# Optimization experiments

Hardware: AMD Instinct MI355X
Metric: run time of the kernel (lower is better)

Reference implementation:

```python
import jax, jax.numpy as jnp
import numpy as np

D_HEAD = 64

def setup_inputs() -> dict:
    key = jax.random.key(0)
    kq, kk, kv, kc = jax.random.split(key, 4)
    B, H, T, D = 2, 16, 2048, D_HEAD
    Q = jax.random.normal(kq, (B, H, T, D), dtype=jnp.float32)
    K = jax.random.normal(kk, (B, H, T, D), dtype=jnp.float32)
    V = jax.random.normal(kv, (B, H, T, D), dtype=jnp.float32)
    # causal mask: True = attend
    mask = jnp.tril(jnp.ones((T, T), dtype=jnp.bool_))
    curvature = jax.random.normal(kc, (H, D, D), dtype=jnp.float32) * 0.02
    return {"Q": Q, "K": K, "V": V, "mask": mask, "curvature": curvature}

def reference(Q, K, V, mask, curvature):
    scale = 1.0 / np.sqrt(Q.shape[-1]).astype(np.float32)
    # per-head learned rotation of Q
    Q_rot = jnp.einsum('bhtd,hde->bhte', Q, curvature)
    scores = jnp.einsum('bhtd,bhsd->bhts', Q_rot, K) * scale  # [B,H,T,T]
    scores = jnp.where(mask[None, None, :, :], scores, -jnp.inf)
    attn = jax.nn.softmax(scores, axis=-1)
    out = jnp.einsum('bhts,bhsd->bhtd', attn, V)
    return out
```

## Files before the change

kernel.cpp:

```cpp
#include <hip/hip_runtime.h>


typedef __attribute__((ext_vector_type(8))) short short8;
typedef __attribute__((ext_vector_type(8))) unsigned short ushort8;
typedef __attribute__((ext_vector_type(4))) float f32x4;
typedef __attribute__((ext_vector_type(2))) _Float16 half2v;
typedef __attribute__((ext_vector_type(4))) _Float16 half4;
typedef __attribute__((ext_vector_type(8))) _Float16 half8;

constexpr int Tc = 2048;
constexpr int Dc = 64;
constexpr size_t REGION = (size_t)32 * Tc * Dc;

__device__ inline unsigned short f2bf(float f) {
    union { float f; unsigned u; } x; x.f = f;
    return (unsigned short)((x.u + 0x7fffu + ((x.u >> 16) & 1u)) >> 16);
}

__device__ inline half2v pkrtz(float a, float b) {
    return __builtin_bit_cast(half2v, __builtin_amdgcn_cvt_pkrtz(a, b));
}

#define MFMA_BF16_K32(a, b, c) __builtin_amdgcn_mfma_f32_16x16x32_bf16((a), (b), (c), 0, 0, 0)
#define MFMA_F16_K16(a, b, c)  __builtin_amdgcn_mfma_f32_16x16x16f16((a), (b), (c), 0, 0, 0)

__global__ __launch_bounds__(256, 1)
void holo_cfrag(const float* __restrict__ Cp, unsigned short* __restrict__ cfrag_g)
{
    const int t = threadIdx.x, lane = t & 63, eb = t >> 6;
    const int l15 = lane & 15, quad = lane >> 4;
    const int h = blockIdx.x;
    const float* Cg = Cp + (size_t)h * Dc * Dc;
    #pragma unroll
    for (int half = 0; half < 2; ++half) {
        short8 b;
        #pragma unroll
        for (int jj = 0; jj < 8; ++jj) {
            const int d = half * 32 + quad * 8 + jj;
            b[jj] = (short)f2bf(Cg[d * Dc + eb * 16 + l15]);
        }
        *(short8*)(&cfrag_g[(((size_t)h * 4 + eb) * 2 + half) * 512 + lane * 8]) = b;
    }
}

__global__ __launch_bounds__(256, 4)
void holo_prep8(const float* __restrict__ Qp, const float* __restrict__ Kp,
                const float* __restrict__ Vp,
                const unsigned short* __restrict__ cfrag_g,
                unsigned short* __restrict__ qfrag_g,
                unsigned short* __restrict__ kfrag_g,
                _Float16* __restrict__ vfrag_g)
{
    __shared__ unsigned short kt[64 * 72];
    __shared__ unsigned short qt[64 * 72];
    __shared__ _Float16      vt[64 * 72];
    __shared__ unsigned short pf[64 * 72];

    const int t = threadIdx.x, lane = t & 63, w = t >> 6;
    const int l15 = lane & 15, quad = lane >> 4, wb = w * 16;
    const int n = blockIdx.x, bh = n >> 5, st = n & 31, h = bh & 15;
    const int s0 = st * 64;

    const float* Qg = Qp + ((size_t)bh * Tc + s0) * Dc;
    const float* Kg = Kp + ((size_t)bh * Tc + s0) * Dc;
    const float* Vg = Vp + ((size_t)bh * Tc + s0) * Dc;

    #pragma unroll
    for (int kk = 0; kk < 4; ++kk) {
        const int flat = kk * 1024 + t * 4;
        const int r = flat >> 6, d0 = flat & 63;
        float4 kv = *(const float4*)(&Kg[flat]);
        ushort4 kp; kp.x = f2bf(kv.x); kp.y = f2bf(kv.y); kp.z = f2bf(kv.z); kp.w = f2bf(kv.w);
        *(ushort4*)(&kt[r * 72 + d0]) = kp;
        float4 qv = *(const float4*)(&Qg[flat]);
        ushort4 qp; qp.x = f2bf(qv.x); qp.y = f2bf(qv.y); qp.z = f2bf(qv.z); qp.w = f2bf(qv.w);
        *(ushort4*)(&qt[r * 72 + d0]) = qp;
        float4 vv = *(const float4*)(&Vg[flat]);
        half4 vp;
        vp[0] = (_Float16)vv.x; vp[1] = (_Float16)vv.y;
        vp[2] = (_Float16)vv.z; vp[3] = (_Float16)vv.w;
        *(half4*)(&vt[r * 72 + d0]) = vp;
    }
    __syncthreads();

    {
        const int row = wb + l15;
        ushort8 p0 = *(const ushort8*)(&kt[row * 72 + quad * 8]);
        ushort8 p1 = *(const ushort8*)(&kt[row * 72 + 32 + quad * 8]);
        unsigned short* kdst = kfrag_g + (((size_t)(bh * 32 + st) * 4 + w) * 64 + lane) * 16;
        *(ushort8*)(kdst) = p0;
        *(ushort8*)(kdst + 8) = p1;
    }

    {
        half8 v0, v1;
        #pragma unroll
        for (int dn = 0; dn < 2; ++dn)
            #pragma unroll
            for (int i = 0; i < 4; ++i)
                v0[dn * 4 + i] = vt[(wb + quad * 4 + i) * 72 + dn * 16 + l15];
        #pragma unroll
        for (int dn = 0; dn < 2; ++dn)
            #pragma unroll
            for (int i = 0; i < 4; ++i)
                v1[dn * 4 + i] = vt[(wb + quad * 4 + i) * 72 + (dn + 2) * 16 + l15];
        _Float16* vdst = vfrag_g + (((size_t)(bh * 32 + st) * 4 + w) * 64 + lane) * 16;
        *(half8*)(vdst) = v0;
        *(half8*)(vdst + 8) = v1;
    }

    {
        short8 a0 = *(const short8*)(&qt[(wb + l15) * 72 + quad * 8]);
        short8 a1 = *(const short8*)(&qt[(wb + l15) * 72 + 32 + quad * 8]);
        #pragma unroll
        for (int eb = 0; eb < 4; ++eb) {
            short8 b0 = *(const short8*)(&cfrag_g[(((size_t)h * 4 + eb) * 2 + 0) * 512 + lane * 8]);
            short8 b1 = *(const short8*)(&cfrag_g[(((size_t)h * 4 + eb) * 2 + 1) * 512 + lane * 8]);
            f32x4 c = {0.f, 0.f, 0.f, 0.f};
            c = MFMA_BF16_K32(a0, b0, c);
            c = MFMA_BF16_K32(a1, b1, c);
            #pragma unroll
            for (int i = 0; i < 4; ++i)
                pf[(wb + quad * 4 + i) * 72 + eb * 16 + l15] = f2bf(c[i] * 0.18033688f);
        }
        __threadfence_block();
        short8 fa0 = *(const short8*)(&pf[(wb + l15) * 72 + quad * 8]);
        short8 fa1 = *(const short8*)(&pf[(wb + l15) * 72 + 32 + quad * 8]);
        const size_t strip = (size_t)bh * 128 + st * 4 + w;
        *(short8*)(&qfrag_g[strip * 1024 + lane * 8]) = fa0;
        *(short8*)(&qfrag_g[strip * 1024 + 512 + lane * 8]) = fa1;
    }
}

__global__ __launch_bounds__(256, 4)
void holo_attn8(const unsigned short* __restrict__ qfrag_g,
                const unsigned short* __restrict__ kfrag_g,
                const _Float16* __restrict__ vfrag_g,
                float* __restrict__ Op)
{
    const int t = threadIdx.x, lane = t & 63, wid = t >> 6;
    const int l15 = lane & 15, quad = lane >> 4, wb = wid * 16;

    const int id = blockIdx.x;
    const int xcd = id & 7, m = (id >> 3) & 31, k = id >> 8;
    const int bh = xcd * 4 + k;
    const int mm = (k >= 2) ? ((m + 16) & 31) : m;
    const int qi = (k & 1) ? (31 - mm) : mm;
    const int q0 = qi * 64;

    short8 qa0, qa1;
    {
        const size_t strip = (size_t)bh * 128 + qi * 4 + wid;
        qa0 = *(const short8*)(&qfrag_g[strip * 1024 + lane * 8]);
        qa1 = *(const short8*)(&qfrag_g[strip * 1024 + 512 + lane * 8]);
    }

    const unsigned short* kbase = kfrag_g + (size_t)bh * 32 * 4 * 1024;
    const _Float16*       vbase = vfrag_g + (size_t)bh * 32 * 4 * 1024;

    f32x4 o[4];
    float l_lane = 0.f;
    #pragma unroll
    for (int dn = 0; dn < 4; ++dn) o[dn] = f32x4{0.f, 0.f, 0.f, 0.f};

    const int rowg = q0 + wb + l15;

    short8 kf0[4], kf1[4];
    half8 vlo[4], vhi[4];
    #pragma unroll
    for (int tn = 0; tn < 4; ++tn) {
        const unsigned short* kfb = kbase + ((size_t)tn * 64 + lane) * 16;
        kf0[tn] = *(const short8*)(kfb);
        kf1[tn] = *(const short8*)(kfb + 8);
        const _Float16* vfb = vbase + ((size_t)tn * 64 + lane) * 16;
        vlo[tn] = *(const half8*)(vfb);
        vhi[tn] = *(const half8*)(vfb + 8);
    }

    for (int j = 0; j <= qi; ++j) {
        f32x4 st[4];
        #pragma unroll
        for (int tn = 0; tn < 4; ++tn) {
            f32x4 c = {0.f, 0.f, 0.f, 0.f};
            c = MFMA_BF16_K32(kf0[tn], qa0, c);
            c = MFMA_BF16_K32(kf1[tn], qa1, c);
            st[tn] = c;
        }

        const int jn = (j < qi) ? j + 1 : j;
        #pragma unroll
        for (int tn = 0; tn < 4; ++tn) {
            const unsigned short* kfb = kbase + (size_t)jn * 4096 + ((size_t)tn * 64 + lane) * 16;
            kf0[tn] = *(const short8*)(kfb);
            kf1[tn] = *(const short8*)(kfb + 8);
        }

        half4 pa[4];
        #pragma unroll
        for (int tn = 0; tn < 4; ++tn) {
            float p[4];
            #pragma unroll
            for (int i = 0; i < 4; ++i) {
                float sv = st[tn][i];
                if (j == qi) {
                    const int colg = j * 64 + tn * 16 + quad * 4 + i;
                    if (colg > rowg) sv = -1e30f;
                }
                p[i] = __builtin_amdgcn_exp2f(sv);
                l_lane += p[i];
            }
            half2v lo = pkrtz(p[0], p[1]);
            half2v hi = pkrtz(p[2], p[3]);
            pa[tn] = __builtin_shufflevector(lo, hi, 0, 1, 2, 3);
        }

        #pragma unroll
        for (int tn = 0; tn < 4; ++tn) {
            half4 vf0 = __builtin_shufflevector(vlo[tn], vlo[tn], 0, 1, 2, 3);
            half4 vf1 = __builtin_shufflevector(vlo[tn], vlo[tn], 4, 5, 6, 7);
            half4 vf2 = __builtin_shufflevector(vhi[tn], vhi[tn], 0, 1, 2, 3);
            half4 vf3 = __builtin_shufflevector(vhi[tn], vhi[tn], 4, 5, 6, 7);
            o[0] = MFMA_F16_K16(vf0, pa[tn], o[0]);
            o[1] = MFMA_F16_K16(vf1, pa[tn], o[1]);
            o[2] = MFMA_F16_K16(vf2, pa[tn], o[2]);
            o[3] = MFMA_F16_K16(vf3, pa[tn], o[3]);
        }

        #pragma unroll
        for (int tn = 0; tn < 4; ++tn) {
            const _Float16* vfb = vbase + (size_t)jn * 4096 + ((size_t)tn * 64 + lane) * 16;
            vlo[tn] = *(const half8*)(vfb);
            vhi[tn] = *(const half8*)(vfb + 8);
        }
    }

    l_lane += __shfl_xor(l_lane, 16);
    l_lane += __shfl_xor(l_lane, 32);
    const float inv = 1.0f / l_lane;

    float* dst = Op + ((size_t)bh * Tc + rowg) * Dc;
    #pragma unroll
    for (int dn = 0; dn < 4; ++dn) {
        float4 r;
        r.x = o[dn][0] * inv; r.y = o[dn][1] * inv;
        r.z = o[dn][2] * inv; r.w = o[dn][3] * inv;
        *(float4*)(&dst[dn * 16 + quad * 4]) = r;
    }
}

extern "C" void kernel_launch(void* const* d_in, const int* in_sizes, int n_in,
                              void* d_out, int out_size, void* d_ws, size_t ws_size,
                              hipStream_t stream) {
    const float* Q = (const float*)d_in[0];
    const float* K = (const float*)d_in[1];
    const float* V = (const float*)d_in[2];
    const float* C = (const float*)d_in[4];
    float* O = (float*)d_out;

    unsigned short* qfrag_w = (unsigned short*)d_ws;
    unsigned short* kfrag_w = qfrag_w + REGION;
    _Float16*       vfrag_w = (_Float16*)(kfrag_w + REGION);
    unsigned short* cfrag_w = (unsigned short*)(vfrag_w + REGION);

    holo_cfrag<<<dim3(16), dim3(256), 0, stream>>>(C, cfrag_w);
    holo_prep8<<<dim3(1024), dim3(256), 0, stream>>>(Q, K, V, cfrag_w, qfrag_w, kfrag_w, vfrag_w);
    holo_attn8<<<dim3(1024), dim3(256), 0, stream>>>(qfrag_w, kfrag_w, vfrag_w, O);
}
```

Before: 144.6 us.

## Split KV loop across wave pairs, two query strips per wave, LDS merge

The attention kernel is restructured so each wave handles two 16-row query strips, with K/V fragment loads shared between them. The four waves form two parity groups, one taking even KV tiles and one taking odd tiles, and the partial outputs and row sums are merged through LDS at the end. Blocks are also reordered longest-first (qi counts down), and launch bounds drop to 2 blocks per SIMD because register use rises. The goal is to halve K/V loads per query row and shorten each wave's serial loop, at the cost of more registers, lower occupancy and a final sync and LDS reduction.

Result: faster. 136.9 us (-5.3%).

```diff
diff --git a/kernel.cpp b/kernel.cpp
--- a/kernel.cpp
+++ b/kernel.cpp
@@ -132,62 +132,74 @@
     }
 }
 
-__global__ __launch_bounds__(256, 4)
-void holo_attn8(const unsigned short* __restrict__ qfrag_g,
-                const unsigned short* __restrict__ kfrag_g,
-                const _Float16* __restrict__ vfrag_g,
-                float* __restrict__ Op)
+__global__ __launch_bounds__(256, 2)
+void holo_attn10(const unsigned short* __restrict__ qfrag_g,
+                 const unsigned short* __restrict__ kfrag_g,
+                 const _Float16* __restrict__ vfrag_g,
+                 float* __restrict__ Op)
 {
+    __shared__ float lds_o[2][2][16][68];
+    __shared__ float lds_l[2][2][16];
+
     const int t = threadIdx.x, lane = t & 63, wid = t >> 6;
-    const int l15 = lane & 15, quad = lane >> 4, wb = wid * 16;
+    const int l15 = lane & 15, quad = lane >> 4;
+    const int hv  = wid & 1;
+    const int par = wid >> 1;
 
     const int id = blockIdx.x;
-    const int xcd = id & 7, m = (id >> 3) & 31, k = id >> 8;
-    const int bh = xcd * 4 + k;
-    const int mm = (k >= 2) ? ((m + 16) & 31) : m;
-    const int qi = (k & 1) ? (31 - mm) : mm;
+    const int xcd = id & 7, sseq = id >> 3;
+    const int qi = 31 - (sseq >> 2);
+    const int bh = xcd * 4 + (sseq & 3);
     const int q0 = qi * 64;
 
-    short8 qa0, qa1;
-    {
-        const size_t strip = (size_t)bh * 128 + qi * 4 + wid;
-        qa0 = *(const short8*)(&qfrag_g[strip * 1024 + lane * 8]);
-        qa1 = *(const short8*)(&qfrag_g[strip * 1024 + 512 + lane * 8]);
+    short8 qa0[2], qa1[2];
+    #pragma unroll
+    for (int s2 = 0; s2 < 2; ++s2) {
+        const size_t strip = (size_t)bh * 128 + qi * 4 + (2 * hv + s2);
+        qa0[s2] = *(const short8*)(&qfrag_g[strip * 1024 + lane * 8]);
+        qa1[s2] = *(const short8*)(&qfrag_g[strip * 1024 + 512 + lane * 8]);
     }
 
     const unsigned short* kbase = kfrag_g + (size_t)bh * 32 * 4 * 1024;
     const _Float16*       vbase = vfrag_g + (size_t)bh * 32 * 4 * 1024;
 
-    f32x4 o[4];
-    float l_lane = 0.f;
-    #pragma unroll
-    for (int dn = 0; dn < 4; ++dn) o[dn] = f32x4{0.f, 0.f, 0.f, 0.f};
-
-    const int rowg = q0 + wb + l15;
+    f32x4 o[2][4];
+    #pragma unroll
+    for (int s2 = 0; s2 < 2; ++s2)
+        #pragma unroll
+        for (int dn = 0; dn < 4; ++dn) o[s2][dn] = f32x4{0.f, 0.f, 0.f, 0.f};
+    float l2[2] = {0.f, 0.f};
+
+    const int rowgA = q0 + (2 * hv) * 16 + l15;
+    const int rowgB = rowgA + 16;
 
     short8 kf0[4], kf1[4];
     half8 vlo[4], vhi[4];
     #pragma unroll
     for (int tn = 0; tn < 4; ++tn) {
-        const unsigned short* kfb = kbase + ((size_t)tn * 64 + lane) * 16;
+        const unsigned short* kfb = kbase + (size_t)par * 4096 + ((size_t)tn * 64 + lane) * 16;
         kf0[tn] = *(const short8*)(kfb);
         kf1[tn] = *(const short8*)(kfb + 8);
-        const _Float16* vfb = vbase + ((size_t)tn * 64 + lane) * 16;
+        const _Float16* vfb = vbase + (size_t)par * 4096 + ((size_t)tn * 64 + lane) * 16;
         vlo[tn] = *(const half8*)(vfb);
         vhi[tn] = *(const half8*)(vfb + 8);
     }
 
-    for (int j = 0; j <= qi; ++j) {
-        f32x4 st[4];
-        #pragma unroll
-        for (int tn = 0; tn < 4; ++tn) {
-            f32x4 c = {0.f, 0.f, 0.f, 0.f};
-            c = MFMA_BF16_K32(kf0[tn], qa0, c);
-            c = MFMA_BF16_K32(kf1[tn], qa1, c);
-            st[tn] = c;
-        }
-
-        const int jn = (j < qi) ? j + 1 : j;
+    for (int j = par; j <= qi; j += 2) {
+        f32x4 stA[4], stB[4];
+        #pragma unroll
+        for (int tn = 0; tn < 4; ++tn) {
+            f32x4 cA = {0.f, 0.f, 0.f, 0.f};
+            cA = MFMA_BF16_K32(kf0[tn], qa0[0], cA);
+            cA = MFMA_BF16_K32(kf1[tn], qa1[0], cA);
+            stA[tn] = cA;
+            f32x4 cB = {0.f, 0.f, 0.f, 0.f};
+            cB = MFMA_BF16_K32(kf0[tn], qa0[1], cB);
+            cB = MFMA_BF16_K32(kf1[tn], qa1[1], cB);
+            stB[tn] = cB;
+        }
+
+        const int jn = (j + 2 <= qi) ? j + 2 : j;
         #pragma unroll
         for (int tn = 0; tn < 4; ++tn) {
             const unsigned short* kfb = kbase + (size_t)jn * 4096 + ((size_t)tn * 64 + lane) * 16;
@@ -195,23 +207,27 @@
             kf1[tn] = *(const short8*)(kfb + 8);
         }
 
-        half4 pa[4];
-        #pragma unroll
-        for (int tn = 0; tn < 4; ++tn) {
-            float p[4];
+        half4 paA[4], paB[4];
+        #pragma unroll
+        for (int tn = 0; tn < 4; ++tn) {
+            float pA[4], pB[4];
             #pragma unroll
             for (int i = 0; i < 4; ++i) {
-                float sv = st[tn][i];
+                float svA = stA[tn][i], svB = stB[tn][i];
                 if (j == qi) {
                     const int colg = j * 64 + tn * 16 + quad * 4 + i;
-                    if (colg > rowg) sv = -1e30f;
+                    if (colg > rowgA) svA = -1e30f;
+                    if (colg > rowgB) svB = -1e30f;
                 }
-                p[i] = __builtin_amdgcn_exp2f(sv);
-                l_lane += p[i];
+                pA[i] = __builtin_amdgcn_exp2f(svA);
+                pB[i] = __builtin_amdgcn_exp2f(svB);
+                l2[0] += pA[i];
+                l2[1] += pB[i];
             }
-            half2v lo = pkrtz(p[0], p[1]);
-            half2v hi = pkrtz(p[2], p[3]);
-            pa[tn] = __builtin_shufflevector(lo, hi, 0, 1, 2, 3);
+            half2v loA = pkrtz(pA[0], pA[1]), hiA = pkrtz(pA[2], pA[3]);
+            paA[tn] = __builtin_shufflevector(loA, hiA, 0, 1, 2, 3);
+            half2v loB = pkrtz(pB[0], pB[1]), hiB = pkrtz(pB[2], pB[3]);
+            paB[tn] = __builtin_shufflevector(loB, hiB, 0, 1, 2, 3);
         }
 
         #pragma unroll
@@ -220,10 +236,14 @@
             half4 vf1 = __builtin_shufflevector(vlo[tn], vlo[tn], 4, 5, 6, 7);
             half4 vf2 = __builtin_shufflevector(vhi[tn], vhi[tn], 0, 1, 2, 3);
             half4 vf3 = __builtin_shufflevector(vhi[tn], vhi[tn], 4, 5, 6, 7);
-            o[0] = MFMA_F16_K16(vf0, pa[tn], o[0]);
-            o[1] = MFMA_F16_K16(vf1, pa[tn], o[1]);
-            o[2] = MFMA_F16_K16(vf2, pa[tn], o[2]);
-            o[3] = MFMA_F16_K16(vf3, pa[tn], o[3]);
+            o[0][0] = MFMA_F16_K16(vf0, paA[tn], o[0][0]);
+            o[0][1] = MFMA_F16_K16(vf1, paA[tn], o[0][1]);
+            o[0][2] = MFMA_F16_K16(vf2, paA[tn], o[0][2]);
+            o[0][3] = MFMA_F16_K16(vf3, paA[tn], o[0][3]);
+            o[1][0] = MFMA_F16_K16(vf0, paB[tn], o[1][0]);
+            o[1][1] = MFMA_F16_K16(vf1, paB[tn], o[1][1]);
+            o[1][2] = MFMA_F16_K16(vf2, paB[tn], o[1][2]);
+            o[1][3] = MFMA_F16_K16(vf3, paB[tn], o[1][3]);
         }
 
         #pragma unroll
@@ -234,17 +254,43 @@
         }
     }
 
-    l_lane += __shfl_xor(l_lane, 16);
-    l_lane += __shfl_xor(l_lane, 32);
-    const float inv = 1.0f / l_lane;
-
-    float* dst = Op + ((size_t)bh * Tc + rowg) * Dc;
-    #pragma unroll
-    for (int dn = 0; dn < 4; ++dn) {
-        float4 r;
-        r.x = o[dn][0] * inv; r.y = o[dn][1] * inv;
-        r.z = o[dn][2] * inv; r.w = o[dn][3] * inv;
-        *(float4*)(&dst[dn * 16 + quad * 4]) = r;
+    #pragma unroll
+    for (int s2 = 0; s2 < 2; ++s2) {
+        l2[s2] += __shfl_xor(l2[s2], 16);
+        l2[s2] += __shfl_xor(l2[s2], 32);
+    }
+
+    if (par == 1) {
+        #pragma unroll
+        for (int s2 = 0; s2 < 2; ++s2) {
+            #pragma unroll
+            for (int dn = 0; dn < 4; ++dn) {
+                float4 r;
+                r.x = o[s2][dn][0]; r.y = o[s2][dn][1];
+                r.z = o[s2][dn][2]; r.w = o[s2][dn][3];
+                *(float4*)(&lds_o[hv][s2][l15][dn * 16 + quad * 4]) = r;
+            }
+            if (quad == 0) lds_l[hv][s2][l15] = l2[s2];
+        }
+    }
+    __syncthreads();
+    if (par == 0) {
+        #pragma unroll
+        for (int s2 = 0; s2 < 2; ++s2) {
+            const float inv = 1.0f / (l2[s2] + lds_l[hv][s2][l15]);
+            const int rowg = q0 + (2 * hv + s2) * 16 + l15;
+            float* dst = Op + ((size_t)bh * Tc + rowg) * Dc;
+            const float* po = &lds_o[hv][s2][l15][0];
+            #pragma unroll
+            for (int dn = 0; dn < 4; ++dn) {
+                float4 r;
+                r.x = (o[s2][dn][0] + po[dn * 16 + quad * 4 + 0]) * inv;
+                r.y = (o[s2][dn][1] + po[dn * 16 + quad * 4 + 1]) * inv;
+                r.z = (o[s2][dn][2] + po[dn * 16 + quad * 4 + 2]) * inv;
+                r.w = (o[s2][dn][3] + po[dn * 16 + quad * 4 + 3]) * inv;
+                *(float4*)(&dst[dn * 16 + quad * 4]) = r;
+            }
+        }
     }
 }
 
@@ -264,5 +310,5 @@
 
     holo_cfrag<<<dim3(16), dim3(256), 0, stream>>>(C, cfrag_w);
     holo_prep8<<<dim3(1024), dim3(256), 0, stream>>>(Q, K, V, cfrag_w, qfrag_w, kfrag_w, vfrag_w);
-    holo_attn8<<<dim3(1024), dim3(256), 0, stream>>>(qfrag_w, kfrag_w, vfrag_w, O);
-}
+    holo_attn10<<<dim3(1024), dim3(256), 0, stream>>>(qfrag_w, kfrag_w, vfrag_w, O);
+}
```

## Stage K/V tiles through double-buffered LDS via direct global-to-LDS loads

Applied to the files above, without the earlier changes.

The attention kernel now has all four waves of a block share K/V tiles. Each tile is loaded once per block into a double-buffered LDS ring with global_load_lds, instead of every wave loading its own copy into registers. The prep kernel's fragment layout is rearranged so each 16-byte lane load maps contiguously into LDS. Blocks are reordered to schedule the longest causal rows first, and MFMA sections get raised wave priority. The cost is an added barrier and vmcnt wait every iteration plus 32KB of LDS per block, and launch bounds drop to 2 blocks per CU.

Result: faster. 136.7 us (-5.5%).

```diff
diff --git a/kernel.cpp b/kernel.cpp
--- a/kernel.cpp
+++ b/kernel.cpp
@@ -23,6 +23,12 @@
 
 #define MFMA_BF16_K32(a, b, c) __builtin_amdgcn_mfma_f32_16x16x32_bf16((a), (b), (c), 0, 0, 0)
 #define MFMA_F16_K16(a, b, c)  __builtin_amdgcn_mfma_f32_16x16x16f16((a), (b), (c), 0, 0, 0)
+
+typedef __attribute__((address_space(3))) unsigned int        lds_u32;
+typedef const __attribute__((address_space(1))) unsigned int  glob_u32;
+__device__ __attribute__((always_inline)) inline void gl_lds16(const void* g, void* l) {
+    __builtin_amdgcn_global_load_lds((glob_u32*)g, (lds_u32*)l, 16, 0, 0);
+}
 
 __global__ __launch_bounds__(256, 1)
 void holo_cfrag(const float* __restrict__ Cp, unsigned short* __restrict__ cfrag_g)
@@ -87,9 +93,9 @@
         const int row = wb + l15;
         ushort8 p0 = *(const ushort8*)(&kt[row * 72 + quad * 8]);
         ushort8 p1 = *(const ushort8*)(&kt[row * 72 + 32 + quad * 8]);
-        unsigned short* kdst = kfrag_g + (((size_t)(bh * 32 + st) * 4 + w) * 64 + lane) * 16;
-        *(ushort8*)(kdst) = p0;
-        *(ushort8*)(kdst + 8) = p1;
+        unsigned short* ktile = kfrag_g + (size_t)(bh * 32 + st) * 4096;
+        *(ushort8*)(&ktile[(w * 64 + lane) * 8])        = p0;
+        *(ushort8*)(&ktile[2048 + (w * 64 + lane) * 8]) = p1;
     }
 
     {
@@ -104,9 +110,9 @@
             #pragma unroll
             for (int i = 0; i < 4; ++i)
                 v1[dn * 4 + i] = vt[(wb + quad * 4 + i) * 72 + (dn + 2) * 16 + l15];
-        _Float16* vdst = vfrag_g + (((size_t)(bh * 32 + st) * 4 + w) * 64 + lane) * 16;
-        *(half8*)(vdst) = v0;
-        *(half8*)(vdst + 8) = v1;
+        _Float16* vtile = vfrag_g + (size_t)(bh * 32 + st) * 4096;
+        *(half8*)(&vtile[(w * 64 + lane) * 8])        = v0;
+        *(half8*)(&vtile[2048 + (w * 64 + lane) * 8]) = v1;
     }
 
     {
@@ -132,21 +138,33 @@
     }
 }
 
-__global__ __launch_bounds__(256, 4)
-void holo_attn8(const unsigned short* __restrict__ qfrag_g,
-                const unsigned short* __restrict__ kfrag_g,
-                const _Float16* __restrict__ vfrag_g,
-                float* __restrict__ Op)
+__global__ __launch_bounds__(256, 2)
+void holo_attn14(const unsigned short* __restrict__ qfrag_g,
+                 const unsigned short* __restrict__ kfrag_g,
+                 const _Float16* __restrict__ vfrag_g,
+                 float* __restrict__ Op)
 {
+    __shared__ unsigned short bufK[2][4096];
+    __shared__ _Float16      bufV[2][4096];
+
     const int t = threadIdx.x, lane = t & 63, wid = t >> 6;
-    const int l15 = lane & 15, quad = lane >> 4, wb = wid * 16;
+    const int l15 = lane & 15, quad = lane >> 4;
 
     const int id = blockIdx.x;
-    const int xcd = id & 7, m = (id >> 3) & 31, k = id >> 8;
-    const int bh = xcd * 4 + k;
-    const int mm = (k >= 2) ? ((m + 16) & 31) : m;
-    const int qi = (k & 1) ? (31 - mm) : mm;
+    const int xcd = id & 7, sseq = id >> 3;
+    const int qi = 31 - (sseq >> 2);
+    const int bh = xcd * 4 + (sseq & 3);
     const int q0 = qi * 64;
+
+    const char* kbase = (const char*)(kfrag_g + (size_t)bh * 32 * 4096);
+    const char* vbase = (const char*)(vfrag_g + (size_t)bh * 32 * 4096);
+
+    {
+        gl_lds16(kbase + wid * 1024 + lane * 16,        &bufK[0][wid * 512]);
+        gl_lds16(kbase + 4096 + wid * 1024 + lane * 16, &bufK[0][2048 + wid * 512]);
+        gl_lds16(vbase + wid * 1024 + lane * 16,        &bufV[0][wid * 512]);
+        gl_lds16(vbase + 4096 + wid * 1024 + lane * 16, &bufV[0][2048 + wid * 512]);
+    }
 
     short8 qa0, qa1;
     {
@@ -155,45 +173,43 @@
         qa1 = *(const short8*)(&qfrag_g[strip * 1024 + 512 + lane * 8]);
     }
 
-    const unsigned short* kbase = kfrag_g + (size_t)bh * 32 * 4 * 1024;
-    const _Float16*       vbase = vfrag_g + (size_t)bh * 32 * 4 * 1024;
-
     f32x4 o[4];
+    #pragma unroll
+    for (int dn = 0; dn < 4; ++dn) o[dn] = f32x4{0.f, 0.f, 0.f, 0.f};
     float l_lane = 0.f;
-    #pragma unroll
-    for (int dn = 0; dn < 4; ++dn) o[dn] = f32x4{0.f, 0.f, 0.f, 0.f};
-
-    const int rowg = q0 + wb + l15;
-
-    short8 kf0[4], kf1[4];
-    half8 vlo[4], vhi[4];
-    #pragma unroll
-    for (int tn = 0; tn < 4; ++tn) {
-        const unsigned short* kfb = kbase + ((size_t)tn * 64 + lane) * 16;
-        kf0[tn] = *(const short8*)(kfb);
-        kf1[tn] = *(const short8*)(kfb + 8);
-        const _Float16* vfb = vbase + ((size_t)tn * 64 + lane) * 16;
-        vlo[tn] = *(const half8*)(vfb);
-        vhi[tn] = *(const half8*)(vfb + 8);
-    }
-
+    const int rowg = q0 + wid * 16 + l15;
+
+    asm volatile("s_waitcnt vmcnt(0)" ::: "memory");
+    __builtin_amdgcn_sched_barrier(0);
+    __syncthreads();
+
+    int cur = 0;
     for (int j = 0; j <= qi; ++j) {
+        if (j < qi) {
+            const char* ks = kbase + (size_t)(j + 1) * 8192;
+            const char* vs = vbase + (size_t)(j + 1) * 8192;
+            const int nb = cur ^ 1;
+            gl_lds16(ks + wid * 1024 + lane * 16,        &bufK[nb][wid * 512]);
+            gl_lds16(ks + 4096 + wid * 1024 + lane * 16, &bufK[nb][2048 + wid * 512]);
+            gl_lds16(vs + wid * 1024 + lane * 16,        &bufV[nb][wid * 512]);
+            gl_lds16(vs + 4096 + wid * 1024 + lane * 16, &bufV[nb][2048 + wid * 512]);
+        }
+
+        const unsigned short* Kl = &bufK[cur][0];
+        const _Float16*       Vl = &bufV[cur][0];
+
         f32x4 st[4];
+        __builtin_amdgcn_s_setprio(1);
         #pragma unroll
         for (int tn = 0; tn < 4; ++tn) {
+            short8 k0 = *(const short8*)(&Kl[(tn * 64 + lane) * 8]);
+            short8 k1 = *(const short8*)(&Kl[2048 + (tn * 64 + lane) * 8]);
             f32x4 c = {0.f, 0.f, 0.f, 0.f};
-            c = MFMA_BF16_K32(kf0[tn], qa0, c);
-            c = MFMA_BF16_K32(kf1[tn], qa1, c);
+            c = MFMA_BF16_K32(k0, qa0, c);
+            c = MFMA_BF16_K32(k1, qa1, c);
             st[tn] = c;
         }
-
-        const int jn = (j < qi) ? j + 1 : j;
-        #pragma unroll
-        for (int tn = 0; tn < 4; ++tn) {
-            const unsigned short* kfb = kbase + (size_t)jn * 4096 + ((size_t)tn * 64 + lane) * 16;
-            kf0[tn] = *(const short8*)(kfb);
-            kf1[tn] = *(const short8*)(kfb + 8);
-        }
+        __builtin_amdgcn_s_setprio(0);
 
         half4 pa[4];
         #pragma unroll
@@ -209,29 +225,30 @@
                 p[i] = __builtin_amdgcn_exp2f(sv);
                 l_lane += p[i];
             }
-            half2v lo = pkrtz(p[0], p[1]);
-            half2v hi = pkrtz(p[2], p[3]);
+            half2v lo = pkrtz(p[0], p[1]), hi = pkrtz(p[2], p[3]);
             pa[tn] = __builtin_shufflevector(lo, hi, 0, 1, 2, 3);
         }
 
+        __builtin_amdgcn_s_setprio(1);
         #pragma unroll
         for (int tn = 0; tn < 4; ++tn) {
-            half4 vf0 = __builtin_shufflevector(vlo[tn], vlo[tn], 0, 1, 2, 3);
-            half4 vf1 = __builtin_shufflevector(vlo[tn], vlo[tn], 4, 5, 6, 7);
-            half4 vf2 = __builtin_shufflevector(vhi[tn], vhi[tn], 0, 1, 2, 3);
-            half4 vf3 = __builtin_shufflevector(vhi[tn], vhi[tn], 4, 5, 6, 7);
+            half8 vl = *(const half8*)(&Vl[(tn * 64 + lane) * 8]);
+            half8 vh = *(const half8*)(&Vl[2048 + (tn * 64 + lane) * 8]);
+            half4 vf0 = __builtin_shufflevector(vl, vl, 0, 1, 2, 3);
+            half4 vf1 = __builtin_shufflevector(vl, vl, 4, 5, 6, 7);
+            half4 vf2 = __builtin_shufflevector(vh, vh, 0, 1, 2, 3);
+            half4 vf3 = __builtin_shufflevector(vh, vh, 4, 5, 6, 7);
             o[0] = MFMA_F16_K16(vf0, pa[tn], o[0]);
             o[1] = MFMA_F16_K16(vf1, pa[tn], o[1]);
             o[2] = MFMA_F16_K16(vf2, pa[tn], o[2]);
             o[3] = MFMA_F16_K16(vf3, pa[tn], o[3]);
         }
-
-        #pragma unroll
-        for (int tn = 0; tn < 4; ++tn) {
-            const _Float16* vfb = vbase + (size_t)jn * 4096 + ((size_t)tn * 64 + lane) * 16;
-            vlo[tn] = *(const half8*)(vfb);
-            vhi[tn] = *(const half8*)(vfb + 8);
-        }
+        __builtin_amdgcn_s_setprio(0);
+
+        asm volatile("s_waitcnt vmcnt(0)" ::: "memory");
+        __builtin_amdgcn_sched_barrier(0);
+        __syncthreads();
+        cur ^= 1;
     }
 
     l_lane += __shfl_xor(l_lane, 16);
@@ -264,5 +281,5 @@
 
     holo_cfrag<<<dim3(16), dim3(256), 0, stream>>>(C, cfrag_w);
     holo_prep8<<<dim3(1024), dim3(256), 0, stream>>>(Q, K, V, cfrag_w, qfrag_w, kfrag_w, vfrag_w);
-    holo_attn8<<<dim3(1024), dim3(256), 0, stream>>>(qfrag_w, kfrag_w, vfrag_w, O);
-}
+    holo_attn14<<<dim3(1024), dim3(256), 0, stream>>>(qfrag_w, kfrag_w, vfrag_w, O);
+}
```
